# Kernel optimization log

Measured on AMD Instinct MI355X. Metric: run time of the kernel, lower is better.

## Reference

```python
import jax, jax.numpy as jnp
import numpy as np

B, S, V, E, R1, R2, L = 16, 128, 32000, 128, 256, 640, 512


def pos_encoding(seq_len, d, n=10000.0):
    # P[k, 2i] = sin(k / n^(2i/d)); P[k, 2i+1] = cos(k / n^(2i/d))
    k = jnp.arange(seq_len, dtype=jnp.float32)[:, None]
    i = jnp.arange(d // 2, dtype=jnp.float32)[None, :]
    ang = k / jnp.power(jnp.float32(n), 2.0 * i / d)
    P = jnp.zeros((seq_len, d), dtype=jnp.float32)
    P = P.at[:, 0::2].set(jnp.sin(ang)).at[:, 1::2].set(jnp.cos(ang))
    return P


def setup_inputs() -> dict:
    key = jax.random.key(0)
    ks = iter(jax.random.split(key, 40))

    def lin(fin, fout):
        W = jax.random.normal(next(ks), (fin, fout), jnp.float32) / np.sqrt(fin)
        b = jax.random.normal(next(ks), (fout,), jnp.float32) * 0.01
        return W, b

    inp = {}
    inp['x'] = jax.random.normal(next(ks), (B, S, V), jnp.float32)
    inp['W_emb'], inp['b_emb'] = lin(V, E)
    inp['W_pos1'], inp['b_pos1'] = lin(2 * E, E)
    inp['W_red'], inp['b_red'] = lin(S * E, R1)
    inp['W_pos2'], inp['b_pos2'] = lin(2 * R1, R1)
    inp['W_red2'], inp['b_red2'] = lin(S * R1, R2)
    inp['W_pos3'], inp['b_pos3'] = lin(2 * R2, R2)
    inp['W_down2'], inp['b_down2'] = lin(R2, L)
    inp['W_flat'], inp['b_flat'] = lin(L * S, L)
    inp['W_d1'], inp['b_d1'] = lin(L, L)
    inp['W_d2'], inp['b_d2'] = lin(L, L)
    inp['W_d3'], inp['b_d3'] = lin(L, L)
    inp['W_p1'], inp['b_p1'] = lin(L, V)
    inp['W_p2'], inp['b_p2'] = lin(L, V)
    return inp


def _square_memory(h):
    # einsum('bij,bkm->bikj') factorizes: out[b,i,k,j] = h[b,i,j] * sum_m h[b,k,m]
    b, s, d = h.shape
    row_sum = h.sum(axis=-1)                       # (B, S)
    q = h[:, :, None, :] * row_sum[:, None, :, None]  # (B, S, S, D)
    return q.reshape(b, s, s * d)


def reference(x, W_emb, b_emb, W_pos1, b_pos1, W_red, b_red, W_pos2, b_pos2,
              W_red2, b_red2, W_pos3, b_pos3, W_down2, b_down2, W_flat, b_flat,
              W_d1, b_d1, W_d2, b_d2, W_d3, b_d3, W_p1, b_p1, W_p2, b_p2):
    relu = jax.nn.relu
    h = relu(x @ W_emb + b_emb)                                  # (B,S,E)
    h = h + relu(pos_encoding(S, 2 * E) @ W_pos1 + b_pos1)
    h = relu(_square_memory(h) @ W_red + b_red)                  # (B,S,R1)
    h = h + relu(pos_encoding(S, 2 * R1) @ W_pos2 + b_pos2)
    h = relu(_square_memory(h) @ W_red2 + b_red2)                # (B,S,R2)
    h = h + relu(pos_encoding(S, 2 * R2) @ W_pos3 + b_pos3)
    h = relu(h @ W_down2 + b_down2)                              # (B,S,L)
    h = relu(h.reshape(h.shape[0], -1) @ W_flat + b_flat)        # (B,L)
    h = relu(h @ W_d1 + b_d1)
    p1 = h @ W_p1 + b_p1
    h = relu(h @ W_d2 + b_d2)
    p2 = h @ W_p2 + b_p2
    h = relu(h @ W_d3 + b_d3)
    p3 = h @ W_p1 + b_p1  # faithful to source: project_1 reused (project_3 unused)
    return p1 + p2 + p3
```

## Files before the change

kernel.cpp:

```cpp
#include <hip/hip_runtime.h>

typedef float  f4   __attribute__((ext_vector_type(4)));
typedef __bf16 bf8_t __attribute__((ext_vector_type(8)));
typedef __bf16 bf4_t __attribute__((ext_vector_type(4)));

__device__ __forceinline__ void glds16(const void* g, void* l) {
    __builtin_amdgcn_global_load_lds(
        (const __attribute__((address_space(1))) void*)g,
        (__attribute__((address_space(3))) void*)l, 16, 0, 0);
}

__global__ __launch_bounds__(256)
void prep_kernel(float* __restrict__ P1, float* __restrict__ P2,
                 float* __restrict__ P3,
                 const float* __restrict__ bp1, const float* __restrict__ bp2,
                 float* __restrict__ bc, float* __restrict__ rs2,
                 const float* __restrict__ Wemb, __bf16* __restrict__ WembT,
                 const float* __restrict__ Wd2, __bf16* __restrict__ Wd2T,
                 const float* __restrict__ Wq1, __bf16* __restrict__ Wq1T,
                 const float* __restrict__ Wq2, __bf16* __restrict__ Wq2T,
                 const float* __restrict__ Wq3, __bf16* __restrict__ Wq3T) {
    const int bid = blockIdx.x;
    const int t = threadIdx.x;
    if (bid < 5280) {
        const float* src; __bf16* dst; int CN, RK, tn, local;
        if (bid < 4000)      { src = Wemb; dst = WembT; RK = 32000; CN = 128; tn = 4;  local = bid; }
        else if (bid < 4320) { src = Wd2;  dst = Wd2T;  RK = 640;   CN = 512; tn = 16; local = bid - 4000; }
        else if (bid < 4352) { src = Wq1;  dst = Wq1T;  RK = 256;   CN = 128; tn = 4;  local = bid - 4320; }
        else if (bid < 4480) { src = Wq2;  dst = Wq2T;  RK = 512;   CN = 256; tn = 8;  local = bid - 4352; }
        else                 { src = Wq3;  dst = Wq3T;  RK = 1280;  CN = 640; tn = 20; local = bid - 4480; }
        const int kt = local / tn, ntl = local - kt * tn;
        const int k0 = kt * 32, n0 = ntl * 32;
        __shared__ float tile[32][33];
        const int r = t >> 3, c4 = (t & 7) * 4;
        const f4 v = *(const f4*)(src + (long)(k0 + r) * CN + n0 + c4);
        tile[r][c4] = v[0]; tile[r][c4 + 1] = v[1];
        tile[r][c4 + 2] = v[2]; tile[r][c4 + 3] = v[3];
        __syncthreads();
        bf4_t o2;
        o2[0] = (__bf16)tile[c4][r];     o2[1] = (__bf16)tile[c4 + 1][r];
        o2[2] = (__bf16)tile[c4 + 2][r]; o2[3] = (__bf16)tile[c4 + 3][r];
        *(bf4_t*)(dst + (long)(n0 + r) * RK + k0 + c4) = o2;
        return;
    }
    int idx = (bid - 5280) * 256 + t;
    const int n1 = 128 * 256, n2 = 128 * 512;
    const int nP = 262144;
    if (idx < nP) {
        float* P; int d, local;
        if (idx < n1)           { P = P1; d = 256;  local = idx; }
        else if (idx < n1 + n2) { P = P2; d = 512;  local = idx - n1; }
        else                    { P = P3; d = 1280; local = idx - n1 - n2; }
        int s = local / d;
        int k = local - s * d;
        int i = k >> 1;
        float ang = (float)s * powf(10000.0f, (-2.0f * (float)i) / (float)d);
        P[local] = (k & 1) ? cosf(ang) : sinf(ang);
    } else if (idx < nP + 32000) {
        int j = idx - nP;
        bc[j] = 2.f * bp1[j] + bp2[j];
    } else if (idx < nP + 32000 + 2048) {
        rs2[idx - nP - 32000] = 0.f;
    }
}

template<int BMODE>
__device__ __forceinline__ void gemm_dev(
    float* As0, float* As1, float* Bb0, float* Bb1,
    const float* __restrict__ A, const void* __restrict__ Bv,
    const void* __restrict__ B2v, float* __restrict__ C,
    const float* __restrict__ bias, const float* __restrict__ addsrc,
    float* __restrict__ rsum,
    int M, int N, int K, int lda, int ldb, int ldc, int kswitch,
    long sA, long sB, long sC, int ksplit, int kchunk, int relu,
    int bn, int bm, int bz) {

    const int t = threadIdx.x;
    const int batch = bz / ksplit;
    const int kz = bz - batch * ksplit;
    const int m0 = bm * 64, n0 = bn * 128;
    const int kb = kz * kchunk;
    const int ke = (kb + kchunk < K) ? (kb + kchunk) : K;
    const int nit = (ke - kb + 31) >> 5;

    const int lane = t & 63;
    const int w = t >> 6;
    const int wm = w >> 1, wn = w & 1;
    const int fr = lane & 15;
    const int fq = (lane >> 4) * 8;

    f4 acc[2][4];
#pragma unroll
    for (int mt = 0; mt < 2; ++mt)
#pragma unroll
        for (int nt = 0; nt < 4; ++nt) acc[mt][nt] = (f4){0.f, 0.f, 0.f, 0.f};

    const float* Ab = A + (long)batch * sA;
    const int mvalid = M - m0;

    const int ra = t >> 3;
    const int ja = (t & 7) ^ (ra & 7);
    const float* aS0 = Ab + (long)(m0 + ra) * lda + 4 * ja;
    const float* aS1 = aS0 + 32L * lda;

    const __bf16* bTS0 = nullptr; const __bf16* bTS1 = nullptr;
    const float* bNS0 = nullptr; const float* bNS2 = nullptr;
    if constexpr (BMODE == 0) {
        const __bf16* BT = (const __bf16*)Bv + (long)batch * sB;
        const int nb = t >> 2;
        const int fb = (nb & 3) ^ ((nb >> 2) & 3);
        const int jb = (t & 3) ^ fb;
        bTS0 = BT + (long)(n0 + nb) * ldb + 8 * jb;
        bTS1 = bTS0 + 64L * ldb;
    } else {
        const float* Bn = (const float*)Bv + (long)batch * sB;
        bNS0 = Bn + (long)(t >> 5) * ldb + n0 + (t & 31) * 4;
        const float* Bn2 = (const float*)(B2v ? B2v : Bv);
        bNS2 = Bn2 + (long)(t >> 5) * ldb + n0 + (t & 31) * 4;
    }

    auto STAGE = [&](float* Ad, float* Bd, int k0) {
        if (ra < mvalid)      glds16(aS0 + k0, Ad + 4 * t);
        if (ra + 32 < mvalid) glds16(aS1 + k0, Ad + 1024 + 4 * t);
        if constexpr (BMODE == 0) {
            glds16(bTS0 + k0, Bd + 4 * t);
            glds16(bTS1 + k0, Bd + 1024 + 4 * t);
        } else {
            const float* bp = (k0 < kswitch) ? (bNS0 + (long)k0 * ldb)
                                             : (bNS2 + (long)(k0 - kswitch) * ldb);
            glds16(bp,             Bd + 4 * t);
            glds16(bp + 8L * ldb,  Bd + 1024 + 4 * t);
            glds16(bp + 16L * ldb, Bd + 2048 + 4 * t);
            glds16(bp + 24L * ldb, Bd + 3072 + 4 * t);
        }
    };

    const int R0 = wm * 32 + fr, R1 = R0 + 16;
    const int jq = (lane >> 4) * 2;
    const int x7 = R0 & 7;
    const int aO00 = R0 * 8 + (jq ^ x7);
    const int aO01 = R0 * 8 + ((jq + 1) ^ x7);
    const int aO10 = R1 * 8 + (jq ^ x7);
    const int aO11 = R1 * 8 + ((jq + 1) ^ x7);
    int bOf[4];
    if constexpr (BMODE == 0) {
        const int fbc = (fr & 3) ^ ((fr >> 2) & 3);
        const int jb2 = (lane >> 4) ^ fbc;
#pragma unroll
        for (int nt = 0; nt < 4; ++nt)
            bOf[nt] = ((wn * 64 + nt * 16 + fr) * 4 + jb2) * 8;
    } else {
#pragma unroll
        for (int nt = 0; nt < 4; ++nt)
            bOf[nt] = wn * 64 + nt * 16 + fr;
    }

    STAGE(As0, Bb0, kb);
    __syncthreads();
    int cur = 0;
    for (int i = 0; i < nit; ++i) {
        const float* Ac = cur ? As1 : As0;
        const float* Bc = cur ? Bb1 : Bb0;
        if (i + 1 < nit) STAGE(cur ? As0 : As1, cur ? Bb0 : Bb1, kb + (i + 1) * 32);

        f4 x0 = *(const f4*)(Ac + aO00 * 4);
        f4 x1 = *(const f4*)(Ac + aO01 * 4);
        f4 x2 = *(const f4*)(Ac + aO10 * 4);
        f4 x3 = *(const f4*)(Ac + aO11 * 4);
        bf8_t af0, af1;
#pragma unroll
        for (int q = 0; q < 4; ++q) {
            af0[q] = (__bf16)x0[q]; af0[4 + q] = (__bf16)x1[q];
            af1[q] = (__bf16)x2[q]; af1[4 + q] = (__bf16)x3[q];
        }
#pragma unroll
        for (int nt = 0; nt < 4; ++nt) {
            bf8_t bv;
            if constexpr (BMODE == 0) {
                bv = *(const bf8_t*)((const __bf16*)Bc + bOf[nt]);
            } else {
                const float* bb = Bc + fq * 128 + bOf[nt];
#pragma unroll
                for (int d2 = 0; d2 < 8; ++d2) bv[d2] = (__bf16)bb[d2 * 128];
            }
            acc[0][nt] = __builtin_amdgcn_mfma_f32_16x16x32_bf16(af0, bv, acc[0][nt], 0, 0, 0);
            acc[1][nt] = __builtin_amdgcn_mfma_f32_16x16x32_bf16(af1, bv, acc[1][nt], 0, 0, 0);
        }
        __syncthreads();
        cur ^= 1;
    }

    float* Cp; long ldcp;
    const bool fin = (ksplit == 1);
    if (!fin) { Cp = C + (long)(batch * ksplit + kz) * M * N; ldcp = N; }
    else      { Cp = C + (long)batch * sC;                    ldcp = ldc; }

    const int rb = m0 + wm * 32 + (lane >> 4) * 4;
    const int cb_ = n0 + wn * 64 + fr;
    float rowpart[2][4] = {{0.f,0.f,0.f,0.f},{0.f,0.f,0.f,0.f}};
#pragma unroll
    for (int mt = 0; mt < 2; ++mt) {
#pragma unroll
        for (int nt = 0; nt < 4; ++nt) {
            const int c = cb_ + nt * 16;
            const float bvl = (fin && bias) ? bias[c] : 0.f;
#pragma unroll
            for (int v = 0; v < 4; ++v) {
                const int r = rb + mt * 16 + v;
                if (r < M) {
                    float val = acc[mt][nt][v] + bvl;
                    if (fin && relu) val = fmaxf(val, 0.f);
                    if (fin && addsrc) val += addsrc[(long)r * ldcp + c];
                    Cp[(long)r * ldcp + c] = val;
                    rowpart[mt][v] += val;
                }
            }
        }
    }
    if (rsum) {
#pragma unroll
        for (int mt = 0; mt < 2; ++mt) {
#pragma unroll
            for (int v = 0; v < 4; ++v) {
                float s = rowpart[mt][v];
                s += __shfl_xor(s, 1); s += __shfl_xor(s, 2);
                s += __shfl_xor(s, 4); s += __shfl_xor(s, 8);
                const int r = rb + mt * 16 + v;
                if (fr == 0 && r < M) atomicAdd(&rsum[(long)bz * M + r], s);
            }
        }
    }
}

template<int BMODE>
__global__ __launch_bounds__(256)
void gemm_v2(const float* A, const void* Bv, const void* B2v, float* C,
             const float* bias, const float* addsrc, float* rsum,
             int M, int N, int K, int lda, int ldb, int ldc, int kswitch,
             long sA, long sB, long sC, int ksplit, int kchunk, int relu) {
    __shared__ __align__(16) float AsF[2][2048];
    __shared__ __align__(16) float Bbuf[2][BMODE ? 4096 : 2048];
    gemm_dev<BMODE>(&AsF[0][0], &AsF[1][0], &Bbuf[0][0], &Bbuf[1][0],
                    A, Bv, B2v, C, bias, addsrc, rsum,
                    M, N, K, lda, ldb, ldc, kswitch, sA, sB, sC,
                    ksplit, kchunk, relu,
                    blockIdx.x, blockIdx.y, blockIdx.z);
}

__global__ __launch_bounds__(256)
void mega1_kernel(const float* __restrict__ x, const __bf16* __restrict__ WembT,
                  float* __restrict__ partG1,
                  const float* __restrict__ P1, const __bf16* __restrict__ Q1T,
                  float* __restrict__ Q1o, const float* __restrict__ bq1,
                  const float* __restrict__ P2, const __bf16* __restrict__ Q2T,
                  float* __restrict__ Q2o, const float* __restrict__ bq2,
                  const float* __restrict__ P3, const __bf16* __restrict__ Q3T,
                  float* __restrict__ Q3o, const float* __restrict__ bq3) {
    __shared__ __align__(16) float AsF[2][2048];
    __shared__ __align__(16) float Bbuf[2][2048];
    float* A0 = &AsF[0][0]; float* A1 = &AsF[1][0];
    float* B0 = &Bbuf[0][0]; float* B1 = &Bbuf[1][0];
    const int bid = blockIdx.x;
    if (bid < 1280) {
        const int xc = bid & 7, j = bid >> 3;
        const int bz = xc + ((j >> 5) << 3);
        const int bm = j & 31;
        gemm_dev<0>(A0, A1, B0, B1, x, WembT, nullptr, partG1,
                    nullptr, nullptr, nullptr,
                    2048, 128, 32000, 32000, 32000, 128, 32000,
                    0, 0, 0, 40, 800, 0, 0, bm, bz);
    } else if (bid < 1282) {
        gemm_dev<0>(A0, A1, B0, B1, P1, Q1T, nullptr, Q1o,
                    bq1, nullptr, nullptr,
                    128, 128, 256, 256, 256, 128, 256,
                    0, 0, 0, 1, 256, 1, 0, bid - 1280, 0);
    } else if (bid < 1286) {
        const int l = bid - 1282;
        gemm_dev<0>(A0, A1, B0, B1, P2, Q2T, nullptr, Q2o,
                    bq2, nullptr, nullptr,
                    128, 256, 512, 512, 512, 256, 512,
                    0, 0, 0, 1, 512, 1, l & 1, l >> 1, 0);
    } else {
        const int l = bid - 1286;
        gemm_dev<0>(A0, A1, B0, B1, P3, Q3T, nullptr, Q3o,
                    bq3, nullptr, nullptr,
                    128, 640, 1280, 1280, 1280, 640, 1280,
                    0, 0, 0, 1, 1280, 1, l % 5, l / 5, 0);
    }
}

__global__ __launch_bounds__(256)
void reduce_splitk(const float* __restrict__ part, float* __restrict__ outp,
                   const float* __restrict__ bias, int MN, int N, int ksplit,
                   int relu) {
    int idx = blockIdx.x * 256 + threadIdx.x;
    if (idx >= MN) return;
    float s = 0.f;
    for (int z = 0; z < ksplit; ++z) s += part[(long)z * MN + idx];
    if (bias) s += bias[idx % N];
    if (relu) s = fmaxf(s, 0.f);
    outp[idx] = s;
}

__global__ __launch_bounds__(256)
void reduce_rs_kernel(const float* __restrict__ part, float* __restrict__ h1,
                      const float* __restrict__ bias, const float* __restrict__ Q1,
                      float* __restrict__ rs1, int ksplit) {
    const int t = threadIdx.x;
    const int idx = blockIdx.x * 256 + t;
    float s = 0.f;
    for (int z = 0; z < ksplit; ++z) s += part[(long)z * 262144 + idx];
    s += bias[idx & 127];
    s = fmaxf(s, 0.f);
    s += Q1[idx & 16383];
    h1[idx] = s;
    float r = s;
    for (int off = 32; off > 0; off >>= 1) r += __shfl_down(r, off, 64);
    __shared__ float p[4];
    const int w = t >> 6, lane = t & 63;
    if (lane == 0) p[w] = r;
    __syncthreads();
    if (t < 2) rs1[(blockIdx.x << 1) + t] = p[t * 2] + p[t * 2 + 1];
}

extern "C" void kernel_launch(void* const* d_in, const int* in_sizes, int n_in,
                              void* d_out, int out_size, void* d_ws, size_t ws_size,
                              hipStream_t stream) {
    const float* x       = (const float*)d_in[0];
    const float* W_emb   = (const float*)d_in[1];
    const float* b_emb   = (const float*)d_in[2];
    const float* W_pos1  = (const float*)d_in[3];
    const float* b_pos1  = (const float*)d_in[4];
    const float* W_red   = (const float*)d_in[5];
    const float* b_red   = (const float*)d_in[6];
    const float* W_pos2  = (const float*)d_in[7];
    const float* b_pos2  = (const float*)d_in[8];
    const float* W_red2  = (const float*)d_in[9];
    const float* b_red2  = (const float*)d_in[10];
    const float* W_pos3  = (const float*)d_in[11];
    const float* b_pos3  = (const float*)d_in[12];
    const float* W_down2 = (const float*)d_in[13];
    const float* b_down2 = (const float*)d_in[14];
    const float* W_flat  = (const float*)d_in[15];
    const float* b_flat  = (const float*)d_in[16];
    const float* W_d1    = (const float*)d_in[17];
    const float* b_d1    = (const float*)d_in[18];
    const float* W_d2    = (const float*)d_in[19];
    const float* b_d2    = (const float*)d_in[20];
    const float* W_d3    = (const float*)d_in[21];
    const float* b_d3    = (const float*)d_in[22];
    const float* W_p1    = (const float*)d_in[23];
    const float* b_p1    = (const float*)d_in[24];
    const float* W_p2    = (const float*)d_in[25];
    const float* b_p2    = (const float*)d_in[26];
    float* out = (float*)d_out;
    float* ws  = (float*)d_ws;

    size_t o = 0;
    auto alloc = [&](size_t n) { size_t p = o; o += (n + 63) & ~(size_t)63; return p; };
    const size_t oP1 = alloc(128 * 256);
    const size_t oP2 = alloc(128 * 512);
    const size_t oP3 = alloc(128 * 1280);
    const size_t oQ1 = alloc(128 * 128);
    const size_t oQ2 = alloc(128 * 256);
    const size_t oQ3 = alloc(128 * 640);
    const size_t oBC = alloc(32000);
    const size_t oH1 = alloc(2048 * 128);
    const size_t oRS1 = alloc(2048);
    const size_t oRS2 = alloc(2048);
    const size_t oH2 = alloc(2048 * 256);
    const size_t oH3 = alloc(2048 * 640);
    const size_t oH4 = alloc(2048 * 512);
    const size_t oH5 = alloc(16 * 512);
    const size_t oH6c = alloc(16 * 1024);
    const size_t oCat = alloc(16 * 1024);
    const size_t oM1 = alloc(16 * 32768);
    const size_t oM2 = alloc(16 * 163840);
    const size_t oWembT = alloc(2048000);
    const size_t oWd2T  = alloc(163840);
    const size_t oQ1T   = alloc(16384);
    const size_t oQ2T   = alloc(65536);
    const size_t oQ3T   = alloc(409600);
    const size_t oRegA = alloc(40u * 262144);
    const size_t oPartG1 = oRegA, oPartF = oRegA, oPartP = oRegA;
    (void)ws_size; (void)in_sizes; (void)n_in; (void)out_size;

    __bf16* WembT = (__bf16*)(ws + oWembT);
    __bf16* Wd2T  = (__bf16*)(ws + oWd2T);
    __bf16* Q1T   = (__bf16*)(ws + oQ1T);
    __bf16* Q2T   = (__bf16*)(ws + oQ2T);
    __bf16* Q3T   = (__bf16*)(ws + oQ3T);

    dim3 blk(256);

    prep_kernel<<<dim3(6437), blk, 0, stream>>>(
        ws + oP1, ws + oP2, ws + oP3, b_p1, b_p2, ws + oBC, ws + oRS2,
        W_emb, WembT, W_down2, Wd2T, W_pos1, Q1T, W_pos2, Q2T, W_pos3, Q3T);
    mega1_kernel<<<dim3(1296), blk, 0, stream>>>(
        x, WembT, ws + oPartG1,
        ws + oP1, Q1T, ws + oQ1, b_pos1,
        ws + oP2, Q2T, ws + oQ2, b_pos2,
        ws + oP3, Q3T, ws + oQ3, b_pos3);
    reduce_rs_kernel<<<dim3(1024), blk, 0, stream>>>(ws + oPartG1, ws + oH1,
                                                     b_emb, ws + oQ1, ws + oRS1, 40);
    gemm_v2<1><<<dim3(256, 1, 1), blk, 0, stream>>>(ws + oRS1, W_red, nullptr,
        ws + oM1, nullptr, nullptr, nullptr,
        16, 32768, 128, 128, 32768, 32768, 1 << 30, 0, 0, 0, 1, 128, 0);
    gemm_v2<1><<<dim3(2, 2, 16), blk, 0, stream>>>(ws + oH1, ws + oM1, nullptr,
        ws + oH2, b_red, ws + oQ2, ws + oRS2,
        128, 256, 128, 128, 256, 256, 1 << 30, 16384, 32768, 32768, 1, 128, 1);
    gemm_v2<1><<<dim3(1280, 1, 1), blk, 0, stream>>>(ws + oRS2, W_red2, nullptr,
        ws + oM2, nullptr, nullptr, nullptr,
        16, 163840, 128, 128, 163840, 163840, 1 << 30, 0, 0, 0, 1, 128, 0);
    gemm_v2<1><<<dim3(5, 2, 16), blk, 0, stream>>>(ws + oH2, ws + oM2, nullptr,
        ws + oH3, b_red2, ws + oQ3, nullptr,
        128, 640, 256, 256, 640, 640, 1 << 30, 32768, 163840, 81920, 1, 256, 1);
    gemm_v2<0><<<dim3(4, 32, 1), blk, 0, stream>>>(ws + oH3, Wd2T, nullptr,
        ws + oH4, b_down2, nullptr, nullptr,
        2048, 512, 640, 640, 640, 512, 1 << 30, 0, 0, 0, 1, 640, 1);
    gemm_v2<1><<<dim3(4, 1, 256), blk, 0, stream>>>(ws + oH4, W_flat, nullptr,
        ws + oPartF, nullptr, nullptr, nullptr,
        16, 512, 65536, 65536, 512, 512, 1 << 30, 0, 0, 0, 256, 256, 0);
    reduce_splitk<<<dim3(32), blk, 0, stream>>>(ws + oPartF, ws + oH5, b_flat,
                                                8192, 512, 256, 1);
    gemm_v2<1><<<dim3(4, 1, 1), blk, 0, stream>>>(ws + oH5, W_d1, nullptr,
        ws + oH6c, b_d1, nullptr, nullptr,
        16, 512, 512, 512, 512, 1024, 1 << 30, 0, 0, 0, 1, 512, 1);
    gemm_v2<1><<<dim3(4, 1, 1), blk, 0, stream>>>(ws + oH6c, W_d2, nullptr,
        ws + oCat + 512, b_d2, nullptr, nullptr,
        16, 512, 512, 1024, 512, 1024, 1 << 30, 0, 0, 0, 1, 512, 1);
    gemm_v2<1><<<dim3(4, 1, 1), blk, 0, stream>>>(ws + oCat + 512, W_d3, nullptr,
        ws + oCat, b_d3, ws + oH6c, nullptr,
        16, 512, 512, 1024, 512, 1024, 1 << 30, 0, 0, 0, 1, 512, 1);
    gemm_v2<1><<<dim3(250, 1, 4), blk, 0, stream>>>(ws + oCat, W_p1, W_p2,
        ws + oPartP, nullptr, nullptr, nullptr,
        16, 32000, 1024, 1024, 32000, 32000, 512, 0, 0, 0, 4, 256, 0);
    reduce_splitk<<<dim3(2000), blk, 0, stream>>>(ws + oPartP, out, ws + oBC,
                                                  512000, 32000, 4, 0);
}
```

Before: 400.0 us.

## Use 128-row tiles for embedding GEMM and cut split-K partials elsewhere

Adds a dedicated 128x128-tile MFMA routine for the large x@W_emb GEMM. Each block loads a 128-row A tile per k-step, so every B tile is reused across twice as many rows, and the K-split changes from 40 to 48 with fewer total blocks. It also reduces the W_flat split-K from 256 to 64 chunks, shrinking the partial buffer and the reduction work. The final projection drops its split-K scratch and reduce kernel in favour of two direct GEMMs, the second adding onto the output of the first. The trade-offs are more LDS per block and fewer, longer-running blocks.

```diff
diff --git a/kernel.cpp b/kernel.cpp
--- a/kernel.cpp
+++ b/kernel.cpp
@@ -232,6 +232,97 @@
     }
 }
 
+__device__ __forceinline__ void gemm1_t128(
+    float* As0, float* As1, float* Bb0, float* Bb1,
+    const float* __restrict__ x, const __bf16* __restrict__ WembT,
+    float* __restrict__ part, int bm, int kz) {
+    const int t = threadIdx.x;
+    const int lane = t & 63;
+    const int w = t >> 6;
+    const int fr = lane & 15;
+    const int m0 = bm * 128;
+    const int kb = kz * 672;
+    const int ke = (kb + 672 < 32000) ? kb + 672 : 32000;
+    const int nit = (ke - kb) >> 5;
+
+    f4 acc[2][8];
+#pragma unroll
+    for (int mt = 0; mt < 2; ++mt)
+#pragma unroll
+        for (int nt = 0; nt < 8; ++nt) acc[mt][nt] = (f4){0.f, 0.f, 0.f, 0.f};
+
+    const int ra = t >> 3;
+    const int ja = (t & 7) ^ (ra & 7);
+    const float* aS = x + (long)(m0 + ra) * 32000 + 4 * ja;
+
+    const int nb = t >> 2;
+    const int fb = (nb & 3) ^ ((nb >> 2) & 3);
+    const int jb = (t & 3) ^ fb;
+    const __bf16* bTS0 = WembT + (long)nb * 32000 + 8 * jb;
+    const __bf16* bTS1 = bTS0 + 64L * 32000;
+
+    auto STAGE = [&](float* Ad, float* Bd, int k0) {
+        glds16(aS + k0,               Ad + 4 * t);
+        glds16(aS + 32L * 32000 + k0, Ad + 1024 + 4 * t);
+        glds16(aS + 64L * 32000 + k0, Ad + 2048 + 4 * t);
+        glds16(aS + 96L * 32000 + k0, Ad + 3072 + 4 * t);
+        glds16(bTS0 + k0, Bd + 4 * t);
+        glds16(bTS1 + k0, Bd + 1024 + 4 * t);
+    };
+
+    const int R0 = w * 32 + fr, R1 = R0 + 16;
+    const int jq = (lane >> 4) * 2;
+    const int x7 = R0 & 7;
+    const int aO00 = R0 * 8 + (jq ^ x7);
+    const int aO01 = R0 * 8 + ((jq + 1) ^ x7);
+    const int aO10 = R1 * 8 + (jq ^ x7);
+    const int aO11 = R1 * 8 + ((jq + 1) ^ x7);
+    const int fbc = (fr & 3) ^ ((fr >> 2) & 3);
+    const int jb2 = (lane >> 4) ^ fbc;
+    int bOf[8];
+#pragma unroll
+    for (int nt = 0; nt < 8; ++nt)
+        bOf[nt] = ((nt * 16 + fr) * 4 + jb2) * 8;
+
+    STAGE(As0, Bb0, kb);
+    __syncthreads();
+    int cur = 0;
+    for (int i = 0; i < nit; ++i) {
+        const float* Ac = cur ? As1 : As0;
+        const float* Bc = cur ? Bb1 : Bb0;
+        if (i + 1 < nit) STAGE(cur ? As0 : As1, cur ? Bb0 : Bb1, kb + (i + 1) * 32);
+
+        f4 x0 = *(const f4*)(Ac + aO00 * 4);
+        f4 x1 = *(const f4*)(Ac + aO01 * 4);
+        f4 x2 = *(const f4*)(Ac + aO10 * 4);
+        f4 x3 = *(const f4*)(Ac + aO11 * 4);
+        bf8_t af0, af1;
+#pragma unroll
+        for (int q = 0; q < 4; ++q) {
+            af0[q] = (__bf16)x0[q]; af0[4 + q] = (__bf16)x1[q];
+            af1[q] = (__bf16)x2[q]; af1[4 + q] = (__bf16)x3[q];
+        }
+#pragma unroll
+        for (int nt = 0; nt < 8; ++nt) {
+            bf8_t bv = *(const bf8_t*)((const __bf16*)Bc + bOf[nt]);
+            acc[0][nt] = __builtin_amdgcn_mfma_f32_16x16x32_bf16(af0, bv, acc[0][nt], 0, 0, 0);
+            acc[1][nt] = __builtin_amdgcn_mfma_f32_16x16x32_bf16(af1, bv, acc[1][nt], 0, 0, 0);
+        }
+        __syncthreads();
+        cur ^= 1;
+    }
+
+    float* Cp = part + (long)kz * 262144;
+    const int rb = m0 + w * 32 + (lane >> 4) * 4;
+#pragma unroll
+    for (int mt = 0; mt < 2; ++mt)
+#pragma unroll
+        for (int nt = 0; nt < 8; ++nt)
+#pragma unroll
+            for (int v = 0; v < 4; ++v)
+                Cp[(long)(rb + mt * 16 + v) * 128 + nt * 16 + fr] = acc[mt][nt][v];
+}
+
 template<int BMODE>
 __global__ __launch_bounds__(256)
 void gemm_v2(const float* A, const void* Bv, const void* B2v, float* C,
@@ -256,32 +347,29 @@
                   float* __restrict__ Q2o, const float* __restrict__ bq2,
                   const float* __restrict__ P3, const __bf16* __restrict__ Q3T,
                   float* __restrict__ Q3o, const float* __restrict__ bq3) {
-    __shared__ __align__(16) float AsF[2][2048];
+    __shared__ __align__(16) float AsF[2][4096];
     __shared__ __align__(16) float Bbuf[2][2048];
     float* A0 = &AsF[0][0]; float* A1 = &AsF[1][0];
     float* B0 = &Bbuf[0][0]; float* B1 = &Bbuf[1][0];
     const int bid = blockIdx.x;
-    if (bid < 1280) {
+    if (bid < 768) {
         const int xc = bid & 7, j = bid >> 3;
-        const int bz = xc + ((j >> 5) << 3);
-        const int bm = j & 31;
-        gemm_dev<0>(A0, A1, B0, B1, x, WembT, nullptr, partG1,
-                    nullptr, nullptr, nullptr,
-                    2048, 128, 32000, 32000, 32000, 128, 32000,
-                    0, 0, 0, 40, 800, 0, 0, bm, bz);
-    } else if (bid < 1282) {
+        const int kz = xc + ((j >> 4) << 3);
+        const int bm = j & 15;
+        gemm1_t128(A0, A1, B0, B1, x, WembT, partG1, bm, kz);
+    } else if (bid < 770) {
         gemm_dev<0>(A0, A1, B0, B1, P1, Q1T, nullptr, Q1o,
                     bq1, nullptr, nullptr,
                     128, 128, 256, 256, 256, 128, 256,
-                    0, 0, 0, 1, 256, 1, 0, bid - 1280, 0);
-    } else if (bid < 1286) {
-        const int l = bid - 1282;
+                    0, 0, 0, 1, 256, 1, 0, bid - 768, 0);
+    } else if (bid < 774) {
+        const int l = bid - 770;
         gemm_dev<0>(A0, A1, B0, B1, P2, Q2T, nullptr, Q2o,
                     bq2, nullptr, nullptr,
                     128, 256, 512, 512, 512, 256, 512,
                     0, 0, 0, 1, 512, 1, l & 1, l >> 1, 0);
     } else {
-        const int l = bid - 1286;
+        const int l = bid - 774;
         gemm_dev<0>(A0, A1, B0, B1, P3, Q3T, nullptr, Q3o,
                     bq3, nullptr, nullptr,
                     128, 640, 1280, 1280, 1280, 640, 1280,
@@ -381,8 +469,8 @@
     const size_t oQ1T   = alloc(16384);
     const size_t oQ2T   = alloc(65536);
     const size_t oQ3T   = alloc(409600);
-    const size_t oRegA = alloc(40u * 262144);
-    const size_t oPartG1 = oRegA, oPartF = oRegA, oPartP = oRegA;
+    const size_t oRegA = alloc(48u * 262144);
+    const size_t oPartG1 = oRegA, oPartF = oRegA;
     (void)ws_size; (void)in_sizes; (void)n_in; (void)out_size;
 
     __bf16* WembT = (__bf16*)(ws + oWembT);
@@ -396,13 +484,13 @@
     prep_kernel<<<dim3(6437), blk, 0, stream>>>(
         ws + oP1, ws + oP2, ws + oP3, b_p1, b_p2, ws + oBC, ws + oRS2,
         W_emb, WembT, W_down2, Wd2T, W_pos1, Q1T, W_pos2, Q2T, W_pos3, Q3T);
-    mega1_kernel<<<dim3(1296), blk, 0, stream>>>(
+    mega1_kernel<<<dim3(784), blk, 0, stream>>>(
         x, WembT, ws + oPartG1,
         ws + oP1, Q1T, ws + oQ1, b_pos1,
         ws + oP2, Q2T, ws + oQ2, b_pos2,
         ws + oP3, Q3T, ws + oQ3, b_pos3);
     reduce_rs_kernel<<<dim3(1024), blk, 0, stream>>>(ws + oPartG1, ws + oH1,
-                                                     b_emb, ws + oQ1, ws + oRS1, 40);
+                                                     b_emb, ws + oQ1, ws + oRS1, 48);
     gemm_v2<1><<<dim3(256, 1, 1), blk, 0, stream>>>(ws + oRS1, W_red, nullptr,
         ws + oM1, nullptr, nullptr, nullptr,
         16, 32768, 128, 128, 32768, 32768, 1 << 30, 0, 0, 0, 1, 128, 0);
@@ -418,11 +506,11 @@
     gemm_v2<0><<<dim3(4, 32, 1), blk, 0, stream>>>(ws + oH3, Wd2T, nullptr,
         ws + oH4, b_down2, nullptr, nullptr,
         2048, 512, 640, 640, 640, 512, 1 << 30, 0, 0, 0, 1, 640, 1);
-    gemm_v2<1><<<dim3(4, 1, 256), blk, 0, stream>>>(ws + oH4, W_flat, nullptr,
+    gemm_v2<1><<<dim3(4, 1, 64), blk, 0, stream>>>(ws + oH4, W_flat, nullptr,
         ws + oPartF, nullptr, nullptr, nullptr,
-        16, 512, 65536, 65536, 512, 512, 1 << 30, 0, 0, 0, 256, 256, 0);
+        16, 512, 65536, 65536, 512, 512, 1 << 30, 0, 0, 0, 64, 1024, 0);
     reduce_splitk<<<dim3(32), blk, 0, stream>>>(ws + oPartF, ws + oH5, b_flat,
-                                                8192, 512, 256, 1);
+                                                8192, 512, 64, 1);
     gemm_v2<1><<<dim3(4, 1, 1), blk, 0, stream>>>(ws + oH5, W_d1, nullptr,
         ws + oH6c, b_d1, nullptr, nullptr,
         16, 512, 512, 512, 512, 1024, 1 << 30, 0, 0, 0, 1, 512, 1);
@@ -432,9 +520,10 @@
     gemm_v2<1><<<dim3(4, 1, 1), blk, 0, stream>>>(ws + oCat + 512, W_d3, nullptr,
         ws + oCat, b_d3, ws + oH6c, nullptr,
         16, 512, 512, 1024, 512, 1024, 1 << 30, 0, 0, 0, 1, 512, 1);
-    gemm_v2<1><<<dim3(250, 1, 4), blk, 0, stream>>>(ws + oCat, W_p1, W_p2,
-        ws + oPartP, nullptr, nullptr, nullptr,
-        16, 32000, 1024, 1024, 32000, 32000, 512, 0, 0, 0, 4, 256, 0);
-    reduce_splitk<<<dim3(2000), blk, 0, stream>>>(ws + oPartP, out, ws + oBC,
-                                                  512000, 32000, 4, 0);
-}
+    gemm_v2<1><<<dim3(250, 1, 1), blk, 0, stream>>>(ws + oCat, W_p1, nullptr,
+        out, ws + oBC, nullptr, nullptr,
+        16, 32000, 512, 1024, 32000, 32000, 1 << 30, 0, 0, 0, 1, 512, 0);
+    gemm_v2<1><<<dim3(250, 1, 1), blk, 0, stream>>>(ws + oCat + 512, W_p2, nullptr,
+        out, nullptr, out, nullptr,
+        16, 32000, 512, 1024, 32000, 32000, 1 << 30, 0, 0, 0, 1, 512, 0);
+}
```

Measured after the change: 373.1 us. 1.07x faster.
